# Kernel tuning notes

Hardware: AMD Instinct MI355X
Metric: run time of the kernel (lower is better)

Reference implementation:

```python
import jax, jax.numpy as jnp
import numpy as np

N_NODES = 50000
N_EDGES = 800000
C = 128
D_IN = 32
T0, T1 = 25000, 25000
OUT = 16


def setup_inputs() -> dict:
    key = jax.random.key(0)
    ks = jax.random.split(key, 16)
    s_in = 1.0 / np.sqrt(D_IN)
    s_c = 1.0 / np.sqrt(C)
    return {
        "feats0": jax.random.normal(ks[0], (T0, D_IN), jnp.float32),
        "feats1": jax.random.normal(ks[1], (T1, D_IN), jnp.float32),
        "enc_w0": jax.random.normal(ks[2], (D_IN, C), jnp.float32) * s_in,
        "enc_b0": jnp.zeros((C,), jnp.float32),
        "enc_w1": jax.random.normal(ks[3], (D_IN, C), jnp.float32) * s_in,
        "enc_b1": jnp.zeros((C,), jnp.float32),
        "w_self0": jax.random.normal(ks[4], (C, C), jnp.float32) * s_c,
        "w_neigh0": jax.random.normal(ks[5], (C, C), jnp.float32) * s_c,
        "b0": jnp.zeros((C,), jnp.float32),
        "w_self1": jax.random.normal(ks[6], (C, C), jnp.float32) * s_c,
        "w_neigh1": jax.random.normal(ks[7], (C, C), jnp.float32) * s_c,
        "b1": jnp.zeros((C,), jnp.float32),
        "head_w": jax.random.normal(ks[8], (C, OUT), jnp.float32) * s_c,
        "head_b": jnp.zeros((OUT,), jnp.float32),
        "node_row_idx": jax.random.randint(ks[9], (N_NODES,), 0, T0 + T1, jnp.int32),
        "edge_index": jax.random.randint(ks[10], (2, N_EDGES), 0, N_NODES, jnp.int32),
    }


def reference(feats0, feats1, enc_w0, enc_b0, enc_w1, enc_b1,
              w_self0, w_neigh0, b0, w_self1, w_neigh1, b1,
              head_w, head_b, node_row_idx, edge_index):
    # Heterogeneous per-table encoding -> [T0+T1, C]
    x0 = feats0 @ enc_w0 + enc_b0
    x1 = feats1 @ enc_w1 + enc_b1
    x_all = jnp.concatenate([x0, x1], axis=0)
    # Irregular gather: each graph node pulls its table row (vectorized form
    # of the Python loop over index_dict/inverse_index_dict in the original)
    x = x_all[node_row_idx]  # [N, C]

    src, dst = edge_index[0], edge_index[1]
    deg = jnp.maximum(
        jax.ops.segment_sum(jnp.ones((N_EDGES,), x.dtype), dst, num_segments=N_NODES),
        1.0)[:, None]

    # GraphSAGE (mean aggr), 2 layers, ReLU between layers
    for ws, wn, bb, act in ((w_self0, w_neigh0, b0, True),
                            (w_self1, w_neigh1, b1, False)):
        agg = jax.ops.segment_sum(x[src], dst, num_segments=N_NODES) / deg
        x = x @ ws + agg @ wn + bb
        if act:
            x = jax.nn.relu(x)

    return x @ head_w + head_b  # [N, OUT]
```

## Files before the change

### kernel.cpp

```cpp
#include <hip/hip_runtime.h>
#include <hip/hip_bf16.h>

#define N_NODES 50000
#define N_EDGES 800000
#define C 128
#define D_IN 32
#define T0 25000
#define OUT_DIM 16
#define NBUCKETS ((N_NODES + 255) / 256)
#define NB1 512
#define CHUNK1 ((N_EDGES + NB1 - 1) / NB1)
#define ENC_BLOCKS 512
#define HIST_BLOCKS 64
#define PREP_ITEMS (2 * 128 * 256 + 2 * 16 * 128)
#define PREP_BLOCKS ((PREP_ITEMS + 255) / 256)


typedef __attribute__((ext_vector_type(8))) short short8;
typedef __attribute__((ext_vector_type(4))) float f32x4;

__device__ __forceinline__ unsigned short f2bf(float f) {
    union { float f; unsigned int i; } u; u.f = f;
    unsigned int x = u.i;
    unsigned int r = x + 0x7fffu + ((x >> 16) & 1u);
    return (unsigned short)(r >> 16);
}
__device__ __forceinline__ float bf2f(unsigned short h) {
    union { unsigned int i; float f; } u; u.i = ((unsigned int)h) << 16;
    return u.f;
}
__device__ __forceinline__ float lo_f(unsigned int w) {
    union { unsigned int i; float f; } u; u.i = w << 16;
    return u.f;
}
__device__ __forceinline__ float hi_f(unsigned int w) {
    union { unsigned int i; float f; } u; u.i = w & 0xffff0000u;
    return u.f;
}
__device__ __forceinline__ void async16(void* lds, const void* g) {
    __builtin_amdgcn_global_load_lds(
        (const __attribute__((address_space(1))) void*)g,
        (__attribute__((address_space(3))) void*)lds, 16, 0, 0);
}
__device__ __forceinline__ void add8(float* a, uint4 v) {
    a[0] += lo_f(v.x); a[1] += hi_f(v.x);
    a[2] += lo_f(v.y); a[3] += hi_f(v.y);
    a[4] += lo_f(v.z); a[5] += hi_f(v.z);
    a[6] += lo_f(v.w); a[7] += hi_f(v.w);
}

__global__ __launch_bounds__(256) void encode_hist_prep_kernel(
    const float* __restrict__ feats0, const float* __restrict__ feats1,
    const float* __restrict__ w0, const float* __restrict__ b0,
    const float* __restrict__ w1, const float* __restrict__ b1,
    const int* __restrict__ row_idx, unsigned short* __restrict__ xh,
    const int* __restrict__ dst, int* __restrict__ hist_out,
    const float* __restrict__ ws0, const float* __restrict__ wn0,
    const float* __restrict__ ws1, const float* __restrict__ wn1,
    const float* __restrict__ hw,
    unsigned short* __restrict__ BT0, unsigned short* __restrict__ BT1,
    unsigned short* __restrict__ hwbh, unsigned short* __restrict__ hwbl)
{
    if (blockIdx.x >= ENC_BLOCKS + HIST_BLOCKS) {
        int idx = (blockIdx.x - ENC_BLOCKS - HIST_BLOCKS) * 256 + threadIdx.x;
        const int per_layer = 128 * 256;
        if (idx < 2 * per_layer) {
            int lyr = idx / per_layer;
            int rem = idx - lyr * per_layer;
            int n = rem >> 8;
            int k = rem & 255;
            int seg = k >> 7;
            int ch = k & 127;
            const float* W = (lyr == 0) ? (seg ? wn0 : ws0)
                                        : (seg ? wn1 : ws1);
            (lyr == 0 ? BT0 : BT1)[(size_t)n * 256 + k] =
                f2bf(W[ch * 128 + n]);
            return;
        }
        int jdx = idx - 2 * per_layer;
        if (jdx >= 2 * 16 * 128) return;
        int plane = jdx >> 11;
        int rem = jdx & 2047;
        int n = rem >> 7;
        int k = rem & 127;
        float v = hw[k * OUT_DIM + n];
        unsigned short hi = f2bf(v);
        (plane ? hwbl : hwbh)[n * 136 + k] = plane ? f2bf(v - bf2f(hi)) : hi;
        return;
    }
    if (blockIdx.x >= ENC_BLOCKS) {
        __shared__ int h[NBUCKETS];
        for (int i = threadIdx.x; i < NBUCKETS; i += 256) h[i] = 0;
        __syncthreads();
        int bid = blockIdx.x - ENC_BLOCKS;
        for (int e = bid * 256 + threadIdx.x; e < N_EDGES;
             e += HIST_BLOCKS * 256)
            atomicAdd(&h[dst[e] >> 8], 1);
        __syncthreads();
        for (int i = threadIdx.x; i < NBUCKETS; i += 256)
            hist_out[bid * NBUCKETS + i] = h[i];
        return;
    }

    __shared__ float sw0[D_IN * C];
    __shared__ float sw1[D_IN * C];
    __shared__ float sb0[C];
    __shared__ float sb1[C];
    for (int i = threadIdx.x; i < D_IN * C; i += blockDim.x) {
        sw0[i] = w0[i];
        sw1[i] = w1[i];
    }
    if (threadIdx.x < C) {
        sb0[threadIdx.x] = b0[threadIdx.x];
        sb1[threadIdx.x] = b1[threadIdx.x];
    }
    __syncthreads();

    const int STEP = ENC_BLOCKS * 16;
    int j = threadIdx.x & 15;
    int ln = threadIdx.x >> 4;
    int n = blockIdx.x * 16 + ln;
    int r = (n < N_NODES) ? row_idx[n] : 0;
    for (; n < N_NODES; n += STEP) {
        int nn = n + STEP;
        int rn = (nn < N_NODES) ? row_idx[nn] : 0;
        const float* f = (r < T0) ? (feats0 + (size_t)r * D_IN)
                                  : (feats1 + (size_t)(r - T0) * D_IN);
        const float* W = (r < T0) ? sw0 : sw1;
        const float* B = (r < T0) ? sb0 : sb1;
        float4 f4[8];
#pragma unroll
        for (int i = 0; i < 8; ++i) f4[i] = ((const float4*)f)[i];
        float acc[8];
#pragma unroll
        for (int cc = 0; cc < 8; ++cc) acc[cc] = B[8 * j + cc];
#pragma unroll
        for (int k = 0; k < D_IN; ++k) {
            float fk = ((const float*)f4)[k];
            float4 wa = *(const float4*)&W[k * C + 8 * j];
            float4 wb = *(const float4*)&W[k * C + 8 * j + 4];
            acc[0] += fk * wa.x; acc[1] += fk * wa.y;
            acc[2] += fk * wa.z; acc[3] += fk * wa.w;
            acc[4] += fk * wb.x; acc[5] += fk * wb.y;
            acc[6] += fk * wb.z; acc[7] += fk * wb.w;
        }
        short8 h8;
#pragma unroll
        for (int cc = 0; cc < 8; ++cc) h8[cc] = (short)f2bf(acc[cc]);
        *(short8*)(xh + (size_t)n * 128 + 8 * j) = h8;
        r = rn;
    }
}

__global__ __launch_bounds__(256) void scanb_kernel(
    const int* __restrict__ hist_out, int* __restrict__ bucket_base,
    int* __restrict__ bucket_cursor, int* __restrict__ offsets)
{
    __shared__ int ws[4];
    int t = threadIdx.x;
    int c = 0;
    if (t < NBUCKETS) {
#pragma unroll 4
        for (int jb = 0; jb < HIST_BLOCKS; ++jb)
            c += hist_out[jb * NBUCKETS + t];
    }
    int lane = t & 63, wid = t >> 6;
    int v = c;
#pragma unroll
    for (int off = 1; off < 64; off <<= 1) {
        int s = __shfl_up(v, off, 64);
        if (lane >= off) v += s;
    }
    if (lane == 63) ws[wid] = v;
    __syncthreads();
    if (t == 0) {
        int run = 0;
#pragma unroll
        for (int jj = 0; jj < 4; ++jj) { int s = ws[jj]; ws[jj] = run; run += s; }
    }
    __syncthreads();
    int excl = ws[wid] + (v - c);
    if (t < NBUCKETS) {
        bucket_base[t] = excl;
        bucket_cursor[t] = excl;
    }
    if (t == 0) {
        bucket_base[NBUCKETS] = N_EDGES;
        offsets[N_NODES] = N_EDGES;
    }
}

__global__ __launch_bounds__(256) void bucket1_kernel(
    const int* __restrict__ src, const int* __restrict__ dst,
    int* __restrict__ bucket_cursor, unsigned int* __restrict__ pairs)
{
    __shared__ int hist[NBUCKETS];
    __shared__ int base[NBUCKETS];
    __shared__ int cur[NBUCKETS];
    int tid = threadIdx.x;
    for (int i = tid; i < NBUCKETS; i += 256) { hist[i] = 0; cur[i] = 0; }
    __syncthreads();
    int ebeg = blockIdx.x * CHUNK1;
    int eend = ebeg + CHUNK1;
    if (eend > N_EDGES) eend = N_EDGES;
    for (int e = ebeg + tid; e < eend; e += 256)
        atomicAdd(&hist[dst[e] >> 8], 1);
    __syncthreads();
    for (int i = tid; i < NBUCKETS; i += 256)
        if (hist[i] > 0) base[i] = atomicAdd(&bucket_cursor[i], hist[i]);
    __syncthreads();
    for (int e = ebeg + tid; e < eend; e += 256) {
        int d = dst[e];
        int b = d >> 8;
        int pos = base[b] + atomicAdd(&cur[b], 1);
        pairs[pos] = ((unsigned)(d & 255) << 16) | (unsigned)src[e];
    }
}

__global__ __launch_bounds__(256) void bucket2_kernel(
    const unsigned int* __restrict__ pairs, const int* __restrict__ bucket_base,
    int* __restrict__ offsets, float* __restrict__ deg,
    unsigned short* __restrict__ src_sorted)
{
    __shared__ int cnt[256];
    __shared__ int noff[256];
    __shared__ int cur[256];
    __shared__ int ws[4];
    int b = blockIdx.x;
    int n0 = b << 8;
    int tid = threadIdx.x;
    int bb = bucket_base[b];
    int be = bucket_base[b + 1];
    cnt[tid] = 0;
    cur[tid] = 0;
    __syncthreads();
    for (int e = bb + tid; e < be; e += 256)
        atomicAdd(&cnt[pairs[e] >> 16], 1);
    __syncthreads();
    int c = cnt[tid];
    int lane = tid & 63, wid = tid >> 6;
    int v = c;
#pragma unroll
    for (int off = 1; off < 64; off <<= 1) {
        int s = __shfl_up(v, off, 64);
        if (lane >= off) v += s;
    }
    if (lane == 63) ws[wid] = v;
    __syncthreads();
    if (tid == 0) {
        int run = 0;
#pragma unroll
        for (int jj = 0; jj < 4; ++jj) { int s = ws[jj]; ws[jj] = run; run += s; }
    }
    __syncthreads();
    int o = bb + ws[wid] + (v - c);
    noff[tid] = o;
    int n = n0 + tid;
    if (n < N_NODES) {
        offsets[n] = o;
        deg[n] = (float)(c > 0 ? c : 1);
    }
    __syncthreads();
    for (int e = bb + tid; e < be; e += 256) {
        unsigned int p = pairs[e];
        int local = p >> 16;
        int pos = noff[local] + atomicAdd(&cur[local], 1);
        src_sorted[pos] = (unsigned short)(p & 0xffffu);
    }
}

__global__ __launch_bounds__(256) void aggregate_kernel(
    const unsigned short* __restrict__ xh, const int* __restrict__ offsets,
    const unsigned short* __restrict__ src_sorted,
    const float* __restrict__ deg, unsigned short* __restrict__ ah)
{
    int wave = (blockIdx.x * blockDim.x + threadIdx.x) >> 6;
    int lane = threadIdx.x & 63;
    if (wave >= N_NODES) return;
    int h = lane >> 4;
    int u = lane & 15;
    int beg = offsets[wave];
    int end = offsets[wave + 1];
    float dgv = deg[wave];
    float acc[8];
#pragma unroll
    for (int j = 0; j < 8; ++j) acc[j] = 0.f;

    for (int e = beg; e < end; e += 16) {
        int s[4];
#pragma unroll
        for (int t = 0; t < 4; ++t) {
            int i2 = e + 4 * t + h;
            s[t] = src_sorted[i2 < end ? i2 : beg];
        }
        uint4 v[4];
#pragma unroll
        for (int t = 0; t < 4; ++t)
            v[t] = *(const uint4*)(xh + (size_t)s[t] * 128 + u * 8);
#pragma unroll
        for (int t = 0; t < 4; ++t)
            if (e + 4 * t + h < end) add8(acc, v[t]);
    }

#pragma unroll
    for (int j = 0; j < 8; ++j) {
        acc[j] += __shfl_xor(acc[j], 16);
        acc[j] += __shfl_xor(acc[j], 32);
    }
    if (lane < 16) {
        float inv = 1.0f / dgv;
        short8 hv;
#pragma unroll
        for (int j = 0; j < 8; ++j)
            hv[j] = (short)f2bf(acc[j] * inv);
        *(short8*)(ah + (size_t)wave * 128 + u * 8) = hv;
    }
}

#define BM 128
__global__ __launch_bounds__(512) void gemm_mfma(
    unsigned short* __restrict__ xh, const unsigned short* __restrict__ ah,
    const unsigned short* __restrict__ BT, const float* __restrict__ bias,
    int mode,
    const unsigned short* __restrict__ hwbh,
    const unsigned short* __restrict__ hwbl,
    const float* __restrict__ hb, float* __restrict__ out)
{
    __shared__ uint4 smem4[4096];
    char* As = (char*)smem4;
    char* Bs = (char*)smem4 + 32768;
    __shared__ float bias_s[C];
    __shared__ unsigned short hwh_s[16 * 136];
    __shared__ unsigned short hwl_s[16 * 136];
    __shared__ float hb_s[OUT_DIM];

    int tid = threadIdx.x;
    int w = tid >> 6, l = tid & 63;
    int row0 = blockIdx.x * BM;
    if (tid < C) bias_s[tid] = bias[tid];
    if (mode == 2) {
        for (int i = tid; i < 16 * 136; i += 512) {
            hwh_s[i] = hwbh[i];
            hwl_s[i] = hwbl[i];
        }
        if (tid < OUT_DIM) hb_s[tid] = hb[tid];
    }

    f32x4 acc[2][4];
#pragma unroll
    for (int mt = 0; mt < 2; ++mt)
#pragma unroll
        for (int nt = 0; nt < 4; ++nt)
            acc[mt][nt] = (f32x4)(0.f);

    int wm = w & 3;
    int wn = w >> 2;
    int quad = l >> 4;
    int mrow = l & 15;

    for (int c = 0; c < 2; ++c) {
        const char* abase = (const char*)(c == 0 ? xh : ah);
#pragma unroll
        for (int i = 0; i < 4; ++i) {
            int off = i * 8192 + tid * 16;
            int rl = off >> 8;
            int row = row0 + rl;
            if (row > N_NODES - 1) row = N_NODES - 1;
            int u = ((off >> 4) & 15) ^ (rl & 15);
            async16(As + off, abase + (size_t)row * 256 + u * 16);
        }
#pragma unroll
        for (int i = 0; i < 4; ++i) {
            int off = i * 8192 + tid * 16;
            int n = off >> 8;
            int u = ((off >> 4) & 15) ^ (n & 15);
            async16(Bs + off, (const char*)BT + (size_t)n * 512 + c * 256 + u * 16);
        }
        __syncthreads();
#pragma unroll
        for (int ks = 0; ks < 4; ++ks) {
            int cu = ks * 4 + quad;
            int swz = (cu ^ mrow) * 16;
            short8 a0 = *(const short8*)(As + (wm * 32 + mrow) * 256 + swz);
            short8 a1 = *(const short8*)(As + (wm * 32 + 16 + mrow) * 256 + swz);
            short8 b[4];
#pragma unroll
            for (int nt = 0; nt < 4; ++nt)
                b[nt] = *(const short8*)(Bs + (wn * 64 + nt * 16 + mrow) * 256 + swz);
#pragma unroll
            for (int nt = 0; nt < 4; ++nt) {
                acc[0][nt] = __builtin_amdgcn_mfma_f32_16x16x32_bf16(a0, b[nt], acc[0][nt], 0, 0, 0);
                acc[1][nt] = __builtin_amdgcn_mfma_f32_16x16x32_bf16(a1, b[nt], acc[1][nt], 0, 0, 0);
            }
        }
        __syncthreads();
    }

    char* th = (char*)smem4;
    int relu = (mode == 1);
#pragma unroll
    for (int mt = 0; mt < 2; ++mt)
#pragma unroll
        for (int nt = 0; nt < 4; ++nt) {
            int col = wn * 64 + nt * 16 + mrow;
#pragma unroll
            for (int r = 0; r < 4; ++r) {
                int rl = wm * 32 + mt * 16 + quad * 4 + r;
                float v = acc[mt][nt][r] + bias_s[col];
                if (relu) v = fmaxf(v, 0.f);
                int su = (col >> 3) ^ (rl & 15);
                *(unsigned short*)(th + rl * 256 + su * 16 + (col & 7) * 2) =
                    f2bf(v);
            }
        }
    __syncthreads();

    if (mode == 1) {
#pragma unroll
        for (int i = 0; i < 4; ++i) {
            int off = i * 8192 + tid * 16;
            int rl = off >> 8;
            int su = (((off >> 4) & 15) ^ (rl & 15)) * 16;
            int row = row0 + rl;
            if (row < N_NODES)
                *(uint4*)((char*)xh + (size_t)row * 256 + (off & 255)) =
                    *(const uint4*)(th + rl * 256 + su);
        }
    } else {
        f32x4 hacc = (f32x4)(0.f);
        const unsigned short* Bp[2] = {hwh_s, hwl_s};
#pragma unroll
        for (int ps = 0; ps < 2; ++ps) {
#pragma unroll
            for (int ks = 0; ks < 4; ++ks) {
                int su = ((ks * 4 + quad) ^ mrow) * 16;
                short8 a = *(const short8*)(th + (w * 16 + mrow) * 256 + su);
                short8 b = *(const short8*)((const char*)Bp[ps] +
                                            mrow * 272 + ks * 64 + quad * 16);
                hacc = __builtin_amdgcn_mfma_f32_16x16x32_bf16(a, b, hacc, 0, 0, 0);
            }
        }
        float bb = hb_s[mrow];
#pragma unroll
        for (int r = 0; r < 4; ++r) {
            int grow = row0 + w * 16 + quad * 4 + r;
            if (grow < N_NODES)
                out[(size_t)grow * OUT_DIM + mrow] = hacc[r] + bb;
        }
    }
}

extern "C" void kernel_launch(void* const* d_in, const int* in_sizes, int n_in,
                              void* d_out, int out_size, void* d_ws, size_t ws_size,
                              hipStream_t stream)
{
    const float* feats0 = (const float*)d_in[0];
    const float* feats1 = (const float*)d_in[1];
    const float* enc_w0 = (const float*)d_in[2];
    const float* enc_b0 = (const float*)d_in[3];
    const float* enc_w1 = (const float*)d_in[4];
    const float* enc_b1 = (const float*)d_in[5];
    const float* w_self0 = (const float*)d_in[6];
    const float* w_neigh0 = (const float*)d_in[7];
    const float* b0 = (const float*)d_in[8];
    const float* w_self1 = (const float*)d_in[9];
    const float* w_neigh1 = (const float*)d_in[10];
    const float* b1 = (const float*)d_in[11];
    const float* head_w = (const float*)d_in[12];
    const float* head_b = (const float*)d_in[13];
    const int* node_row_idx = (const int*)d_in[14];
    const int* edge_index = (const int*)d_in[15];
    const int* e_src = edge_index;
    const int* e_dst = edge_index + N_EDGES;

    char* p = (char*)d_ws;
    unsigned short* xh = (unsigned short*)p;  p += (size_t)N_NODES * C * 2;
    unsigned short* ah = (unsigned short*)p;  p += (size_t)N_NODES * C * 2;
    unsigned short* BT0 = (unsigned short*)p; p += (size_t)128 * 256 * 2;
    unsigned short* BT1 = (unsigned short*)p; p += (size_t)128 * 256 * 2;
    unsigned short* hwbh = (unsigned short*)p; p += (size_t)16 * 136 * 2;
    unsigned short* hwbl = (unsigned short*)p; p += (size_t)16 * 136 * 2;
    float* deg = (float*)p;        p += (size_t)N_NODES * 4;
    int* offsets = (int*)p;        p += (size_t)(N_NODES + 8) * 4;
    int* hist_out = (int*)p;       p += (size_t)(HIST_BLOCKS * NBUCKETS + 8) * 4;
    int* bucket_base = (int*)p;    p += (size_t)(NBUCKETS + 8) * 4;
    int* bucket_cursor = (int*)p;  p += (size_t)(NBUCKETS + 8) * 4;
    unsigned short* src_sorted = (unsigned short*)p;
    p += (size_t)N_EDGES * 2;
    unsigned int* pairs = (unsigned int*)ah;

    encode_hist_prep_kernel<<<ENC_BLOCKS + HIST_BLOCKS + PREP_BLOCKS, 256, 0,
                              stream>>>(
        feats0, feats1, enc_w0, enc_b0, enc_w1, enc_b1, node_row_idx, xh,
        e_dst, hist_out,
        w_self0, w_neigh0, w_self1, w_neigh1, head_w, BT0, BT1, hwbh, hwbl);

    scanb_kernel<<<1, 256, 0, stream>>>(hist_out, bucket_base,
                                        bucket_cursor, offsets);
    bucket1_kernel<<<NB1, 256, 0, stream>>>(e_src, e_dst, bucket_cursor, pairs);
    bucket2_kernel<<<NBUCKETS, 256, 0, stream>>>(pairs, bucket_base, offsets,
                                                 deg, src_sorted);

    aggregate_kernel<<<(N_NODES * 64 + 255) / 256, 256, 0, stream>>>(
        xh, offsets, src_sorted, deg, ah);
    gemm_mfma<<<(N_NODES + BM - 1) / BM, 512, 0, stream>>>(
        xh, ah, BT0, b0, 1, hwbh, hwbl, head_b, (float*)d_out);

    aggregate_kernel<<<(N_NODES * 64 + 255) / 256, 256, 0, stream>>>(
        xh, offsets, src_sorted, deg, ah);
    gemm_mfma<<<(N_NODES + BM - 1) / BM, 512, 0, stream>>>(
        xh, ah, BT1, b1, 2, hwbh, hwbl, head_b, (float*)d_out);
}
```

Before: 229.0 us.

## Fuse neighbor aggregation into the SAGE GEMM kernel with ping-pong feature buffers

Merges the separate aggregate kernel into the MFMA GEMM kernel. Each 512-thread block gathers and mean-aggregates neighbor features for its 128 rows straight into shared memory, while the self features and both weight halves are loaded asynchronously. This avoids writing the aggregated matrix to global memory and reading it back, and removes two launches. Layer outputs now alternate between two buffers so that in-place writes cannot race with other blocks' gathers. The cost is much more shared memory per block (about 128KB+), which lowers occupancy for the latency-bound gather. The gather loop is also deeper (8 loads in flight instead of 4).

```diff
diff --git a/kernel.cpp b/kernel.cpp
--- a/kernel.cpp
+++ b/kernel.cpp
@@ -269,66 +269,21 @@
     }
 }
 
-__global__ __launch_bounds__(256) void aggregate_kernel(
-    const unsigned short* __restrict__ xh, const int* __restrict__ offsets,
+#define BM 128
+__global__ __launch_bounds__(512) void fused_agg_gemm(
+    const unsigned short* __restrict__ IN, unsigned short* __restrict__ OUTP,
+    const int* __restrict__ offsets,
     const unsigned short* __restrict__ src_sorted,
-    const float* __restrict__ deg, unsigned short* __restrict__ ah)
-{
-    int wave = (blockIdx.x * blockDim.x + threadIdx.x) >> 6;
-    int lane = threadIdx.x & 63;
-    if (wave >= N_NODES) return;
-    int h = lane >> 4;
-    int u = lane & 15;
-    int beg = offsets[wave];
-    int end = offsets[wave + 1];
-    float dgv = deg[wave];
-    float acc[8];
-#pragma unroll
-    for (int j = 0; j < 8; ++j) acc[j] = 0.f;
-
-    for (int e = beg; e < end; e += 16) {
-        int s[4];
-#pragma unroll
-        for (int t = 0; t < 4; ++t) {
-            int i2 = e + 4 * t + h;
-            s[t] = src_sorted[i2 < end ? i2 : beg];
-        }
-        uint4 v[4];
-#pragma unroll
-        for (int t = 0; t < 4; ++t)
-            v[t] = *(const uint4*)(xh + (size_t)s[t] * 128 + u * 8);
-#pragma unroll
-        for (int t = 0; t < 4; ++t)
-            if (e + 4 * t + h < end) add8(acc, v[t]);
-    }
-
-#pragma unroll
-    for (int j = 0; j < 8; ++j) {
-        acc[j] += __shfl_xor(acc[j], 16);
-        acc[j] += __shfl_xor(acc[j], 32);
-    }
-    if (lane < 16) {
-        float inv = 1.0f / dgv;
-        short8 hv;
-#pragma unroll
-        for (int j = 0; j < 8; ++j)
-            hv[j] = (short)f2bf(acc[j] * inv);
-        *(short8*)(ah + (size_t)wave * 128 + u * 8) = hv;
-    }
-}
-
-#define BM 128
-__global__ __launch_bounds__(512) void gemm_mfma(
-    unsigned short* __restrict__ xh, const unsigned short* __restrict__ ah,
+    const float* __restrict__ deg,
     const unsigned short* __restrict__ BT, const float* __restrict__ bias,
     int mode,
     const unsigned short* __restrict__ hwbh,
     const unsigned short* __restrict__ hwbl,
     const float* __restrict__ hb, float* __restrict__ out)
 {
-    __shared__ uint4 smem4[4096];
-    char* As = (char*)smem4;
-    char* Bs = (char*)smem4 + 32768;
+    __shared__ char As[32768];
+    __shared__ char Bs[65536];
+    __shared__ char Ah[32768];
     __shared__ float bias_s[C];
     __shared__ unsigned short hwh_s[16 * 136];
     __shared__ unsigned short hwl_s[16 * 136];
@@ -346,6 +301,71 @@
         if (tid < OUT_DIM) hb_s[tid] = hb[tid];
     }
 
+#pragma unroll
+    for (int i = 0; i < 4; ++i) {
+        int off = i * 8192 + tid * 16;
+        int rl = off >> 8;
+        int row = row0 + rl;
+        if (row > N_NODES - 1) row = N_NODES - 1;
+        int u = ((off >> 4) & 15) ^ (rl & 15);
+        async16(As + off, (const char*)IN + (size_t)row * 256 + u * 16);
+    }
+#pragma unroll
+    for (int i = 0; i < 8; ++i) {
+        int off2 = i * 8192 + tid * 16;
+        int cc = off2 >> 15;
+        int off = off2 & 32767;
+        int n = off >> 8;
+        int u = ((off >> 4) & 15) ^ (n & 15);
+        async16(Bs + off2, (const char*)BT + (size_t)n * 512 + cc * 256 + u * 16);
+    }
+
+    int h = l >> 4;
+    int u16 = l & 15;
+    for (int k = 0; k < 16; ++k) {
+        int rl = w * 16 + k;
+        int node = row0 + rl;
+        int beg = 0, end = 0;
+        float dgv = 1.f;
+        if (node < N_NODES) {
+            beg = offsets[node];
+            end = offsets[node + 1];
+            dgv = deg[node];
+        }
+        float acc8[8];
+#pragma unroll
+        for (int j = 0; j < 8; ++j) acc8[j] = 0.f;
+        for (int e = beg; e < end; e += 32) {
+            int s[8];
+#pragma unroll
+            for (int t = 0; t < 8; ++t) {
+                int i2 = e + 4 * t + h;
+                s[t] = src_sorted[i2 < end ? i2 : beg];
+            }
+            uint4 v[8];
+#pragma unroll
+            for (int t = 0; t < 8; ++t)
+                v[t] = *(const uint4*)(IN + (size_t)s[t] * 128 + u16 * 8);
+#pragma unroll
+            for (int t = 0; t < 8; ++t)
+                if (e + 4 * t + h < end) add8(acc8, v[t]);
+        }
+#pragma unroll
+        for (int j = 0; j < 8; ++j) {
+            acc8[j] += __shfl_xor(acc8[j], 16);
+            acc8[j] += __shfl_xor(acc8[j], 32);
+        }
+        if (l < 16) {
+            float inv = 1.0f / dgv;
+            short8 hv;
+#pragma unroll
+            for (int j = 0; j < 8; ++j)
+                hv[j] = (short)f2bf(acc8[j] * inv);
+            *(short8*)(Ah + rl * 256 + ((u16 ^ (rl & 15)) * 16)) = hv;
+        }
+    }
+    __syncthreads();
+
     f32x4 acc[2][4];
 #pragma unroll
     for (int mt = 0; mt < 2; ++mt)
@@ -358,45 +378,30 @@
     int quad = l >> 4;
     int mrow = l & 15;
 
-    for (int c = 0; c < 2; ++c) {
-        const char* abase = (const char*)(c == 0 ? xh : ah);
-#pragma unroll
-        for (int i = 0; i < 4; ++i) {
-            int off = i * 8192 + tid * 16;
-            int rl = off >> 8;
-            int row = row0 + rl;
-            if (row > N_NODES - 1) row = N_NODES - 1;
-            int u = ((off >> 4) & 15) ^ (rl & 15);
-            async16(As + off, abase + (size_t)row * 256 + u * 16);
-        }
-#pragma unroll
-        for (int i = 0; i < 4; ++i) {
-            int off = i * 8192 + tid * 16;
-            int n = off >> 8;
-            int u = ((off >> 4) & 15) ^ (n & 15);
-            async16(Bs + off, (const char*)BT + (size_t)n * 512 + c * 256 + u * 16);
-        }
-        __syncthreads();
+#pragma unroll
+    for (int cch = 0; cch < 2; ++cch) {
+        const char* Ab = cch ? Ah : As;
+        const char* Bb = Bs + cch * 32768;
 #pragma unroll
         for (int ks = 0; ks < 4; ++ks) {
             int cu = ks * 4 + quad;
             int swz = (cu ^ mrow) * 16;
-            short8 a0 = *(const short8*)(As + (wm * 32 + mrow) * 256 + swz);
-            short8 a1 = *(const short8*)(As + (wm * 32 + 16 + mrow) * 256 + swz);
+            short8 a0 = *(const short8*)(Ab + (wm * 32 + mrow) * 256 + swz);
+            short8 a1 = *(const short8*)(Ab + (wm * 32 + 16 + mrow) * 256 + swz);
             short8 b[4];
 #pragma unroll
             for (int nt = 0; nt < 4; ++nt)
-                b[nt] = *(const short8*)(Bs + (wn * 64 + nt * 16 + mrow) * 256 + swz);
+                b[nt] = *(const short8*)(Bb + (wn * 64 + nt * 16 + mrow) * 256 + swz);
 #pragma unroll
             for (int nt = 0; nt < 4; ++nt) {
                 acc[0][nt] = __builtin_amdgcn_mfma_f32_16x16x32_bf16(a0, b[nt], acc[0][nt], 0, 0, 0);
                 acc[1][nt] = __builtin_amdgcn_mfma_f32_16x16x32_bf16(a1, b[nt], acc[1][nt], 0, 0, 0);
             }
         }
-        __syncthreads();
-    }
-
-    char* th = (char*)smem4;
+    }
+    __syncthreads();
+
+    char* th = As;
     int relu = (mode == 1);
 #pragma unroll
     for (int mt = 0; mt < 2; ++mt)
@@ -423,7 +428,7 @@
             int su = (((off >> 4) & 15) ^ (rl & 15)) * 16;
             int row = row0 + rl;
             if (row < N_NODES)
-                *(uint4*)((char*)xh + (size_t)row * 256 + (off & 255)) =
+                *(uint4*)((char*)OUTP + (size_t)row * 256 + (off & 255)) =
                     *(const uint4*)(th + rl * 256 + su);
         }
     } else {
@@ -475,7 +480,7 @@
 
     char* p = (char*)d_ws;
     unsigned short* xh = (unsigned short*)p;  p += (size_t)N_NODES * C * 2;
-    unsigned short* ah = (unsigned short*)p;  p += (size_t)N_NODES * C * 2;
+    unsigned short* xh2 = (unsigned short*)p; p += (size_t)N_NODES * C * 2;
     unsigned short* BT0 = (unsigned short*)p; p += (size_t)128 * 256 * 2;
     unsigned short* BT1 = (unsigned short*)p; p += (size_t)128 * 256 * 2;
     unsigned short* hwbh = (unsigned short*)p; p += (size_t)16 * 136 * 2;
@@ -487,7 +492,7 @@
     int* bucket_cursor = (int*)p;  p += (size_t)(NBUCKETS + 8) * 4;
     unsigned short* src_sorted = (unsigned short*)p;
     p += (size_t)N_EDGES * 2;
-    unsigned int* pairs = (unsigned int*)ah;
+    unsigned int* pairs = (unsigned int*)xh2;
 
     encode_hist_prep_kernel<<<ENC_BLOCKS + HIST_BLOCKS + PREP_BLOCKS, 256, 0,
                               stream>>>(
@@ -501,13 +506,11 @@
     bucket2_kernel<<<NBUCKETS, 256, 0, stream>>>(pairs, bucket_base, offsets,
                                                  deg, src_sorted);
 
-    aggregate_kernel<<<(N_NODES * 64 + 255) / 256, 256, 0, stream>>>(
-        xh, offsets, src_sorted, deg, ah);
-    gemm_mfma<<<(N_NODES + BM - 1) / BM, 512, 0, stream>>>(
-        xh, ah, BT0, b0, 1, hwbh, hwbl, head_b, (float*)d_out);
-
-    aggregate_kernel<<<(N_NODES * 64 + 255) / 256, 256, 0, stream>>>(
-        xh, offsets, src_sorted, deg, ah);
-    gemm_mfma<<<(N_NODES + BM - 1) / BM, 512, 0, stream>>>(
-        xh, ah, BT1, b1, 2, hwbh, hwbl, head_b, (float*)d_out);
-}
+    int ngrid = (N_NODES + BM - 1) / BM;
+    fused_agg_gemm<<<ngrid, 512, 0, stream>>>(
+        xh, xh2, offsets, src_sorted, deg, BT0, b0, 1,
+        hwbh, hwbl, head_b, (float*)d_out);
+    fused_agg_gemm<<<ngrid, 512, 0, stream>>>(
+        xh2, xh, offsets, src_sorted, deg, BT1, b1, 2,
+        hwbh, hwbl, head_b, (float*)d_out);
+}
```

Result: slower. 300.8 us (+31.4%).
